# Optimization experiments

Measured on AMD Instinct MI355X. Metric: run time of the kernel, lower is better.

Reference implementation:

```python
import jax, jax.numpy as jnp
import numpy as np


def setup_inputs() -> dict:
    key = jax.random.key(0)
    k1, k2 = jax.random.split(key)
    N, M, D = 16384, 16384, 3
    src_V = jax.random.normal(k1, (N, D), dtype=jnp.float32)
    tar_V = jax.random.normal(k2, (M, D), dtype=jnp.float32)
    return {"src_V": src_V, "tar_V": tar_V}


def reference(src_V, tar_V):
    # 1-NN: for each target point find nearest source point (replaces cKDTree).
    # Squared distances via ||t||^2 - 2 t.s + ||s||^2 ; [M, N]
    d2 = (
        jnp.sum(tar_V * tar_V, axis=1, keepdims=True)
        - 2.0 * (tar_V @ src_V.T)
        + jnp.sum(src_V * src_V, axis=1)[None, :]
    )
    ii = jnp.argmin(d2, axis=1)            # [M] nearest src index per target
    diff = src_V[ii] - tar_V               # [M, 3]
    loss = 0.5 * jnp.sum(diff * diff)
    return loss
```

## Files before the change

kernel.cpp:

```cpp
#include <hip/hip_runtime.h>
#include <math.h>

constexpr int N_SRC = 16384;
constexpr int M_TAR = 16384;

constexpr int BLOCKS = M_TAR / 32;
constexpr int TPB = 1024;
constexpr int CHUNKS = 256;
constexpr int TILE = 4096;
constexpr int TILES = N_SRC / TILE;
constexpr int IPT = TILE / CHUNKS / 2;

__global__ void zero_out(float* __restrict__ out) {
    if (threadIdx.x == 0) out[0] = 0.0f;
}

__device__ __forceinline__ float embed_ao(float t, unsigned mask_v, unsigned row_s) {
    float r;
    asm("v_and_or_b32 %0, %1, %2, %3"
        : "=v"(r) : "v"(t), "v"(mask_v), "s"(row_s));
    return r;
}
__device__ __forceinline__ void min3(float& b, float e0, float e1) {
    asm("v_min3_f32 %0, %1, %2, %3"
        : "=v"(b) : "v"(b), "v"(e0), "v"(e1));
}

__global__ __launch_bounds__(TPB, 8) void nn6(const float* __restrict__ src,
                                              const float* __restrict__ tar,
                                              float* __restrict__ out) {
    __shared__ float4 tile[TILE];

    const int tid   = threadIdx.x;
    const int g     = tid & 3;
    const int chunk = tid >> 2;
    const int tbase = blockIdx.x * 32;

    float txm2[8], tym2[8], tzm2[8], best[8];
#pragma unroll
    for (int k = 0; k < 8; ++k) {
        int T = tbase + g + 4 * k;
        txm2[k] = -2.0f * tar[3 * T + 0];
        tym2[k] = -2.0f * tar[3 * T + 1];
        tzm2[k] = -2.0f * tar[3 * T + 2];
        best[k] = INFINITY;
    }

    unsigned mask_v = 0xFFFFFFC0u;

    for (int tl = 0; tl < TILES; ++tl) {
#pragma unroll
        for (int r = 0; r < TILE / TPB; ++r) {
            int p  = tid + r * TPB;
            int j3 = 3 * (tl * TILE + p);
            float x = src[j3 + 0], y = src[j3 + 1], z = src[j3 + 2];
            tile[p] = make_float4(x, y, z, fmaf(x, x, fmaf(y, y, z * z)));
        }
        __syncthreads();

#pragma unroll
        for (int i = 0; i < IPT; ++i) {
            float4 s0 = tile[(2 * i + 0) * CHUNKS + chunk];
            float4 s1 = tile[(2 * i + 1) * CHUNKS + chunk];
            unsigned row0 = (unsigned)(tl * 2 * IPT + 2 * i + 0);
            unsigned row1 = (unsigned)(tl * 2 * IPT + 2 * i + 1);
#pragma unroll
            for (int k = 0; k < 8; ++k) {
                float t0 = fmaf(s0.z, tzm2[k], s0.w);
                t0 = fmaf(s0.y, tym2[k], t0);
                t0 = fmaf(s0.x, txm2[k], t0);
                float t1 = fmaf(s1.z, tzm2[k], s1.w);
                t1 = fmaf(s1.y, tym2[k], t1);
                t1 = fmaf(s1.x, txm2[k], t1);
                float e0 = embed_ao(t0, mask_v, row0);
                float e1 = embed_ao(t1, mask_v, row1);
                min3(best[k], e0, e1);
            }
        }
        __syncthreads();
    }

    float* fv = (float*)tile;
    int*   fj = (int*)tile + 32 * 256;
#pragma unroll
    for (int k = 0; k < 8; ++k) {
        unsigned b = __float_as_uint(best[k]);
        int j  = (int)((b & 63u) * CHUNKS + chunk);
        int lt = g + 4 * k;
        fv[lt * CHUNKS + chunk] = __uint_as_float(b & 0xFFFFFFC0u);
        fj[lt * CHUNKS + chunk] = j;
    }
    __syncthreads();

    const int tprime = tid >> 5;
    const int sub    = tid & 31;
    float bv = fv[tprime * CHUNKS + sub];
    int   bj = fj[tprime * CHUNKS + sub];
#pragma unroll
    for (int m = 1; m < 8; ++m) {
        float v = fv[tprime * CHUNKS + sub + 32 * m];
        int   j = fj[tprime * CHUNKS + sub + 32 * m];
        if (v < bv) { bv = v; bj = j; }
    }
#pragma unroll
    for (int s = 16; s >= 1; s >>= 1) {
        float vv = __shfl_xor(bv, s, 64);
        int   jj = __shfl_xor(bj, s, 64);
        if (vv < bv) { bv = vv; bj = jj; }
    }
    __syncthreads();

    if (sub == 0) {
        int tt = tbase + tprime;
        float dx = src[3 * bj + 0] - tar[3 * tt + 0];
        float dy = src[3 * bj + 1] - tar[3 * tt + 1];
        float dz = src[3 * bj + 2] - tar[3 * tt + 2];
        fv[tprime] = 0.5f * fmaf(dx, dx, fmaf(dy, dy, dz * dz));
    }
    __syncthreads();
    if (tid == 0) {
        float ssum = 0.0f;
#pragma unroll
        for (int i = 0; i < 32; ++i) ssum += fv[i];
        atomicAdd(out, ssum);
    }
}

extern "C" void kernel_launch(void* const* d_in, const int* in_sizes, int n_in,
                              void* d_out, int out_size, void* d_ws, size_t ws_size,
                              hipStream_t stream) {
    const float* src = (const float*)d_in[0];
    const float* tar = (const float*)d_in[1];
    float* out = (float*)d_out;
    (void)d_ws; (void)ws_size;

    zero_out<<<1, 64, 0, stream>>>(out);
    nn6<<<BLOCKS, TPB, 0, stream>>>(src, tar, out);
}
```

Measured before the change: 90.19 us.

## Double-buffer source tiles in LDS with register prefetch of next tile

Halves the tile size and adds a second LDS buffer. The next tile's source points are loaded into registers before the current tile is processed, then written to the alternate buffer afterwards, so global-load latency overlaps compute and only one barrier is needed per tile. The tile loop is fully unrolled and the min3 asm is rewritten with an in-place operand. This costs extra registers for the prefetched values plus more tile iterations, and with 1024-thread blocks register pressure or the larger unroll could reduce occupancy.

```diff
diff --git a/kernel.cpp b/kernel.cpp
--- a/kernel.cpp
+++ b/kernel.cpp
@@ -7,9 +7,10 @@
 constexpr int BLOCKS = M_TAR / 32;
 constexpr int TPB = 1024;
 constexpr int CHUNKS = 256;
-constexpr int TILE = 4096;
+constexpr int TILE = 2048;
 constexpr int TILES = N_SRC / TILE;
-constexpr int IPT = TILE / CHUNKS / 2;
+constexpr int ROWS_PT = TILE / CHUNKS;
+constexpr int IPT = ROWS_PT / 2;
 
 __global__ void zero_out(float* __restrict__ out) {
     if (threadIdx.x == 0) out[0] = 0.0f;
@@ -22,14 +23,14 @@
     return r;
 }
 __device__ __forceinline__ void min3(float& b, float e0, float e1) {
-    asm("v_min3_f32 %0, %1, %2, %3"
-        : "=v"(b) : "v"(b), "v"(e0), "v"(e1));
+    asm("v_min3_f32 %0, %0, %1, %2"
+        : "+v"(b) : "v"(e0), "v"(e1));
 }
 
-__global__ __launch_bounds__(TPB, 8) void nn6(const float* __restrict__ src,
+__global__ __launch_bounds__(TPB, 8) void nn7(const float* __restrict__ src,
                                               const float* __restrict__ tar,
                                               float* __restrict__ out) {
-    __shared__ float4 tile[TILE];
+    __shared__ float4 tile[2 * TILE];
 
     const int tid   = threadIdx.x;
     const int g     = tid & 3;
@@ -46,24 +47,36 @@
         best[k] = INFINITY;
     }
 
+    {
+        const float* q0 = src + 3 * tid;
+        const float* q1 = src + 3 * (tid + TPB);
+        float x0 = q0[0], y0 = q0[1], z0 = q0[2];
+        float x1 = q1[0], y1 = q1[1], z1 = q1[2];
+        tile[tid]       = make_float4(x0, y0, z0, fmaf(x0, x0, fmaf(y0, y0, z0 * z0)));
+        tile[tid + TPB] = make_float4(x1, y1, z1, fmaf(x1, x1, fmaf(y1, y1, z1 * z1)));
+    }
+    __syncthreads();
+
     unsigned mask_v = 0xFFFFFFC0u;
 
+#pragma unroll
     for (int tl = 0; tl < TILES; ++tl) {
-#pragma unroll
-        for (int r = 0; r < TILE / TPB; ++r) {
-            int p  = tid + r * TPB;
-            int j3 = 3 * (tl * TILE + p);
-            float x = src[j3 + 0], y = src[j3 + 1], z = src[j3 + 2];
-            tile[p] = make_float4(x, y, z, fmaf(x, x, fmaf(y, y, z * z)));
+        float x0, y0, z0, x1, y1, z1;
+        if (tl + 1 < TILES) {
+            const float* q0 = src + 3 * ((tl + 1) * TILE + tid);
+            const float* q1 = q0 + 3 * TPB;
+            x0 = q0[0]; y0 = q0[1]; z0 = q0[2];
+            x1 = q1[0]; y1 = q1[1]; z1 = q1[2];
+            __builtin_amdgcn_sched_barrier(0);
         }
-        __syncthreads();
 
+        const int cb = (tl & 1) * TILE;
 #pragma unroll
         for (int i = 0; i < IPT; ++i) {
-            float4 s0 = tile[(2 * i + 0) * CHUNKS + chunk];
-            float4 s1 = tile[(2 * i + 1) * CHUNKS + chunk];
-            unsigned row0 = (unsigned)(tl * 2 * IPT + 2 * i + 0);
-            unsigned row1 = (unsigned)(tl * 2 * IPT + 2 * i + 1);
+            float4 s0 = tile[cb + (2 * i + 0) * CHUNKS + chunk];
+            float4 s1 = tile[cb + (2 * i + 1) * CHUNKS + chunk];
+            unsigned row0 = (unsigned)(tl * ROWS_PT + 2 * i + 0);
+            unsigned row1 = row0 + 1;
 #pragma unroll
             for (int k = 0; k < 8; ++k) {
                 float t0 = fmaf(s0.z, tzm2[k], s0.w);
@@ -76,6 +89,12 @@
                 float e1 = embed_ao(t1, mask_v, row1);
                 min3(best[k], e0, e1);
             }
+        }
+
+        if (tl + 1 < TILES) {
+            const int wb = ((tl + 1) & 1) * TILE;
+            tile[wb + tid]       = make_float4(x0, y0, z0, fmaf(x0, x0, fmaf(y0, y0, z0 * z0)));
+            tile[wb + tid + TPB] = make_float4(x1, y1, z1, fmaf(x1, x1, fmaf(y1, y1, z1 * z1)));
         }
         __syncthreads();
     }
@@ -135,5 +154,5 @@
     (void)d_ws; (void)ws_size;
 
     zero_out<<<1, 64, 0, stream>>>(out);
-    nn6<<<BLOCKS, TPB, 0, stream>>>(src, tar, out);
+    nn7<<<BLOCKS, TPB, 0, stream>>>(src, tar, out);
 }
```

After: 86.05 us. 1.05x faster.
